# Kernel optimization log

Hardware: AMD Instinct MI355X
Metric: run time of the kernel (lower is better)

The kernel has to match this reference:

```python
import jax, jax.numpy as jnp
import numpy as np

N = 20480          # total points (single cloud, batch id 0)
C = 64             # in_channels
K = 16             # neighbors
CHUNK = 512        # knn_batch_size: query chunk for cdist
BN_EPS = 1e-5
# grid_size_options: [tower, background, line] x 3 axes
GRID_OPTIONS = np.array([[0.05, 0.05, 0.05],
                         [0.20, 0.20, 0.20],
                         [0.10, 0.10, 0.10]], dtype=np.float32)


def setup_inputs() -> dict:
    key = jax.random.key(0)
    k1, k2, k3, k4 = jax.random.split(key, 4)
    feat = jax.random.normal(k1, (N, C), jnp.float32)
    coord = jax.random.uniform(k2, (N, 3), jnp.float32)
    batch = jnp.zeros((N,), jnp.int32)
    fj_w1 = jax.random.normal(k3, (C, 32), jnp.float32) * 0.05
    fj_b1 = jnp.zeros((32,), jnp.float32)
    bn_gamma = jnp.ones((32,), jnp.float32)
    bn_beta = jnp.zeros((32,), jnp.float32)
    fj_w2 = jax.random.normal(k4, (32, 3), jnp.float32) * 0.05
    fj_b2 = jnp.zeros((3,), jnp.float32)
    return {"feat": feat, "coord": coord, "batch": batch,
            "fj_w1": fj_w1, "fj_b1": fj_b1, "bn_gamma": bn_gamma,
            "bn_beta": bn_beta, "fj_w2": fj_w2, "fj_b2": fj_b2}


def reference(feat, coord, batch, fj_w1, fj_b1, bn_gamma, bn_beta, fj_w2, fj_b2):
    # ---- chunked brute-force KNN (cdist + topk, self excluded) ----
    sq_all = jnp.sum(coord * coord, axis=-1)            # [N]
    col = jnp.arange(N)
    coords_chunks = coord.reshape(-1, CHUNK, 3)
    idx_chunks = jnp.arange(N).reshape(-1, CHUNK)

    def knn_chunk(args):
        cq, qi = args                                   # [CHUNK,3], [CHUNK]
        d2 = (jnp.sum(cq * cq, -1)[:, None] + sq_all[None, :]
              - 2.0 * (cq @ coord.T))                   # [CHUNK, N]
        d2 = jnp.maximum(d2, 1e-12)
        d2 = jnp.where(col[None, :] == qi[:, None], jnp.inf, d2)
        neg, idx = jax.lax.top_k(-d2, K)                # smallest-K (sqrt monotone)
        return jnp.sqrt(-neg), idx

    dists, idxs = jax.lax.map(jax.checkpoint(knn_chunk), (coords_chunks, idx_chunks))
    all_dist = dists.reshape(N, K)                      # [N, K]
    all_idx = idxs.reshape(N, K)                        # [N, K]

    # ---- per-point covariance of neighbor coords + 3x3 SVD (local PCA) ----
    nb = coord[all_idx]                                 # [N, K, 3]
    nc = nb - nb.mean(axis=1, keepdims=True)
    cov = jnp.einsum('nkd,nke->nde', nc, nc) / (K - 1)  # [N, 3, 3]
    S = jnp.linalg.svd(cov, compute_uv=False)           # descending, [N, 3]
    S_norm = S / (S.sum(axis=1, keepdims=True) + 1e-6)
    linearity = (S_norm[:, 0] - (S_norm[:, 1] + S_norm[:, 2]))[:, None]  # [N,1]

    mean_dist = all_dist.mean(axis=1, keepdims=True)
    density = 1.0 / (mean_dist + 1e-6)

    # ---- feature_judge MLP: Linear -> BatchNorm1d (train stats) -> ReLU -> Linear ----
    h = feat @ fj_w1 + fj_b1
    mu = h.mean(axis=0)
    var = h.var(axis=0)  # biased, as torch BN uses for normalization
    h = (h - mu) / jnp.sqrt(var + BN_EPS) * bn_gamma + bn_beta
    h = jax.nn.relu(h)
    probs = jax.nn.softmax(h @ fj_w2 + fj_b2, axis=1)   # [N, 3]

    tower_prob = (density * 2.0 + probs[:, 0:1]) / 3.0
    background_prob = (jnp.maximum(1.0 - linearity, 1.0 - density) + probs[:, 1:2]) / 3.0
    line_prob = (linearity * 2.0 + probs[:, 2:3]) / 3.0

    go = jnp.asarray(GRID_OPTIONS)
    line_grid = go[2] * jnp.array([1.0, 1.0, 5.0], jnp.float32)  # z-axis line grid *5
    grids = (tower_prob * go[0][None, :] + background_prob * go[1][None, :]
             + line_prob * line_grid[None, :] + 1e-6)   # [N, 3]
    return grids
```

## Files before the change

### kernel.cpp

```cpp
#include <hip/hip_runtime.h>

#define NPTS   20480
#define KNN    16
#define NSLOT  20
#define NCH    32
#define NFEAT  64
#define BN_EPS 1e-5f
#define AMB_EPS 2.6e-7f
#define GH     16
#define NCELL  (GH*GH*GH)
#define RHO0   2
#define NBLK   (NPTS / 256)
#define MLPBLK (NPTS / 32)
#define NGRP   (NPTS / 64)
#define NWAVE  4
#define NPAR   4

__device__ __forceinline__ unsigned med3u(unsigned a, unsigned b, unsigned c) {
    unsigned d;
    asm("v_med3_u32 %0, %1, %2, %3" : "=v"(d) : "v"(a), "v"(b), "v"(c));
    return d;
}

__device__ __forceinline__ float ref_d2_raw(float qx, float qy, float qz, float sqq,
                                            float cx, float cy, float cz, float sqc) {
    float dot = fmaf(qz, cz, fmaf(qy, cy, __fmul_rn(qx, cx)));
    float t   = __fadd_rn(sqq, sqc);
    return fmaf(-2.0f, dot, t);
}
__device__ __forceinline__ float ref_d2(float qx, float qy, float qz, float sqq,
                                        float cx, float cy, float cz, float sqc) {
    return fmaxf(ref_d2_raw(qx, qy, qz, sqq, cx, cy, cz, sqc), 1e-12f);
}

template <int STEP>
__device__ __forceinline__ void scan_range(const float4* __restrict__ spts,
                                           int c0, int c1, float4 qp, int self,
                                           unsigned* b) {
    for (int c = c0; c < c1; c += STEP) {
        float4 s = spts[c];
        float d2 = ref_d2_raw(qp.x, qp.y, qp.z, qp.w, s.x, s.y, s.z, s.w);
        unsigned key = (__float_as_uint(d2) & 0xFFFF8000u) | (unsigned)c;
        if (c == self) key = 0xFFFFFFFFu;
#pragma unroll
        for (int s2 = NSLOT - 1; s2 >= 1; --s2) b[s2] = med3u(key, b[s2 - 1], b[s2]);
        b[0] = min(key, b[0]);
    }
}

__global__ __launch_bounds__(256) void zero_cells(int* __restrict__ p) {
    p[blockIdx.x * 256 + threadIdx.x] = 0;
}

__global__ __launch_bounds__(256) void prep_mlp(const float* __restrict__ coord,
                                                float4* __restrict__ pts4,
                                                int* __restrict__ pcell,
                                                int* __restrict__ cnt,
                                                const float* __restrict__ feat,
                                                const float* __restrict__ w1,
                                                const float* __restrict__ b1,
                                                float* __restrict__ h_ws,
                                                float* __restrict__ partials) {
    if (blockIdx.x < NBLK) {
        int i = blockIdx.x * 256 + threadIdx.x;
        float x = coord[3 * i + 0], y = coord[3 * i + 1], z = coord[3 * i + 2];
        float sq = __fadd_rn(__fadd_rn(__fmul_rn(x, x), __fmul_rn(y, y)),
                             __fmul_rn(z, z));
        pts4[i] = make_float4(x, y, z, sq);
        int ix = min(GH - 1, max(0, (int)(x * (float)GH)));
        int iy = min(GH - 1, max(0, (int)(y * (float)GH)));
        int iz = min(GH - 1, max(0, (int)(z * (float)GH)));
        int cell = (iz * GH + iy) * GH + ix;
        pcell[i] = cell;
        atomicAdd(&cnt[cell], 1);
        return;
    }
    const int tid  = threadIdx.x;
    const int blk2 = blockIdx.x - NBLK;
    const int lane = tid & 63;
    const int wv   = tid >> 6;
    const int pt   = blk2 * 32 + (tid >> 3);
    const int k0   = (tid & 7) * 8;

    float h[NCH];
#pragma unroll
    for (int j = 0; j < NCH; ++j) h[j] = 0.f;
    const float4* f4 = reinterpret_cast<const float4*>(feat + (size_t)pt * NFEAT + k0);
#pragma unroll
    for (int c4 = 0; c4 < 2; ++c4) {
        float4 f = f4[c4];
        float fv[4] = {f.x, f.y, f.z, f.w};
#pragma unroll
        for (int e = 0; e < 4; ++e) {
            int c = k0 + c4 * 4 + e;
#pragma unroll
            for (int j = 0; j < NCH; ++j)
                h[j] = fmaf(fv[e], w1[c * NCH + j], h[j]);
        }
    }
#pragma unroll
    for (int j = 0; j < NCH; ++j) {
        h[j] += __shfl_xor(h[j], 1, 64);
        h[j] += __shfl_xor(h[j], 2, 64);
        h[j] += __shfl_xor(h[j], 4, 64);
        h[j] += b1[j];
    }
    if ((tid & 7) == 0) {
        float4* hd = reinterpret_cast<float4*>(h_ws + (size_t)pt * NCH);
#pragma unroll
        for (int j4 = 0; j4 < NCH / 4; ++j4)
            hd[j4] = make_float4(h[j4 * 4], h[j4 * 4 + 1],
                                 h[j4 * 4 + 2], h[j4 * 4 + 3]);
    }
    __shared__ float redS[4][NCH];
    __shared__ float redQ[4][NCH];
#pragma unroll
    for (int j = 0; j < NCH; ++j) {
        bool holder = (lane & 7) == 0;
        float v  = holder ? h[j] : 0.f;
        float vv = holder ? h[j] * h[j] : 0.f;
#pragma unroll
        for (int off = 8; off < 64; off <<= 1) {
            v  += __shfl_xor(v,  off, 64);
            vv += __shfl_xor(vv, off, 64);
        }
        if (lane == 0) { redS[wv][j] = v; redQ[wv][j] = vv; }
    }
    __syncthreads();
    if (tid < 64) {
        int j = tid;
        float r;
        if (j < NCH) r = redS[0][j] + redS[1][j] + redS[2][j] + redS[3][j];
        else {
            int jj = j - NCH;
            r = redQ[0][jj] + redQ[1][jj] + redQ[2][jj] + redQ[3][jj];
        }
        partials[blk2 * 64 + j] = r;
    }
}

__global__ __launch_bounds__(256) void scatter_pref(const float4* __restrict__ pts4,
                                                    const int* __restrict__ pcell,
                                                    const int* __restrict__ cnt,
                                                    int* __restrict__ cursor,
                                                    float4* __restrict__ spts,
                                                    int* __restrict__ sidx,
                                                    const float* __restrict__ partials,
                                                    float* __restrict__ mustats,
                                                    int* __restrict__ startArr) {
    const int tid = threadIdx.x;
    const int lane = tid & 63;
    if (blockIdx.x < NBLK) {
        __shared__ int chunks[256];
        __shared__ int sstart[NCELL];
        int local[16];
        int base = tid * 16, s = 0;
#pragma unroll
        for (int i = 0; i < 16; ++i) { local[i] = cnt[base + i]; s += local[i]; }
        chunks[tid] = s;
        __syncthreads();
        if (tid < 64) {
            int a0 = chunks[4 * tid + 0], a1 = chunks[4 * tid + 1];
            int a2 = chunks[4 * tid + 2], a3 = chunks[4 * tid + 3];
            int tot = a0 + a1 + a2 + a3;
            int inc = tot;
#pragma unroll
            for (int d = 1; d < 64; d <<= 1) {
                int t = __shfl_up(inc, d, 64);
                if (lane >= d) inc += t;
            }
            int excl = inc - tot;
            chunks[4 * tid + 0] = excl;
            chunks[4 * tid + 1] = excl + a0;
            chunks[4 * tid + 2] = excl + a0 + a1;
            chunks[4 * tid + 3] = excl + a0 + a1 + a2;
        }
        __syncthreads();
        int acc = chunks[tid];
#pragma unroll
        for (int i = 0; i < 16; ++i) { sstart[base + i] = acc; acc += local[i]; }
        __syncthreads();
        int i = blockIdx.x * 256 + tid;
        int c = pcell[i];
        int slot = sstart[c] + atomicAdd(&cursor[c], 1);
        spts[slot] = pts4[i];
        sidx[slot] = i;
        return;
    }
    if (tid < 64) {
        double s = 0.0;
        for (int bk = 0; bk < MLPBLK; ++bk) s += (double)partials[bk * 64 + lane];
        __shared__ double smu[NCH];
        if (lane < NCH) { double mu = s / (double)NPTS; smu[lane] = mu; mustats[lane] = (float)mu; }
        __syncthreads();
        if (lane >= NCH) {
            int jj = lane - NCH;
            double var = s / (double)NPTS - smu[jj] * smu[jj];
            mustats[lane] = (float)(1.0 / sqrt(var + (double)BN_EPS));
        }
    } else if (tid < 128) {
        __syncthreads();
        int base = lane * (NCELL / 64);
        int tot = 0;
        for (int i = 0; i < NCELL / 64; ++i) tot += cnt[base + i];
        int inc = tot;
#pragma unroll
        for (int d = 1; d < 64; d <<= 1) {
            int t = __shfl_up(inc, d, 64);
            if (lane >= d) inc += t;
        }
        int acc = inc - tot;
        for (int i = 0; i < NCELL / 64; ++i) { startArr[base + i] = acc; acc += cnt[base + i]; }
        if (lane == 63) startArr[NCELL] = acc;
    } else {
        __syncthreads();
    }
}

__global__ __launch_bounds__(256) void knn_scan(
    const float4* __restrict__ spts, const int* __restrict__ start,
    unsigned* __restrict__ quarterkeys) {
    __shared__ unsigned keysh[NWAVE * NSLOT][64];
    const int lane = threadIdx.x & 63;
    const int wv   = threadIdx.x >> 6;
    const int g    = blockIdx.x >> 2;
    const int par  = blockIdx.x & 3;
    const int slot = g * 64 + lane;
    const float4 qp = spts[slot];
    const int ix = min(GH - 1, max(0, (int)(qp.x * (float)GH)));
    const int iy = min(GH - 1, max(0, (int)(qp.y * (float)GH)));
    const int iz = min(GH - 1, max(0, (int)(qp.z * (float)GH)));

    unsigned b[NSLOT];
#pragma unroll
    for (int s = 0; s < NSLOT; ++s) b[s] = 0xFFFFFFFFu;
    {
        const int zlo = max(0, iz - RHO0), zhi = min(GH - 1, iz + RHO0);
        const int ylo = max(0, iy - RHO0), yhi = min(GH - 1, iy + RHO0);
        const int xlo = max(0, ix - RHO0), xhi = min(GH - 1, ix + RHO0);
        int r = 0;
        for (int cz = zlo; cz <= zhi; ++cz)
            for (int cy = ylo; cy <= yhi; ++cy) {
                if ((r & (NWAVE - 1)) == wv) {
                    const int rb = (cz * GH + cy) * GH;
                    int c0 = start[rb + xlo];
                    int c1 = start[rb + xhi + 1];
                    scan_range<NPAR>(spts, c0 + ((par - c0) & (NPAR - 1)), c1,
                                     qp, slot, b);
                }
                ++r;
            }
    }
#pragma unroll
    for (int s = 0; s < NSLOT; ++s) keysh[wv * NSLOT + s][lane] = b[s];
    __syncthreads();

    unsigned m[NSLOT];
    if (wv < 2) {
#pragma unroll
        for (int s = 0; s < NSLOT; ++s) m[s] = 0xFFFFFFFFu;
        for (int p2 = 2 * wv; p2 <= 2 * wv + 1; ++p2) {
#pragma unroll
            for (int s = 0; s < NSLOT; ++s) {
                unsigned key = keysh[p2 * NSLOT + s][lane];
#pragma unroll
                for (int t = NSLOT - 1; t >= 1; --t) m[t] = med3u(key, m[t - 1], m[t]);
                m[0] = min(key, m[0]);
            }
        }
    }
    __syncthreads();
    if (wv < 2) {
#pragma unroll
        for (int s = 0; s < NSLOT; ++s) keysh[wv * NSLOT + s][lane] = m[s];
    }
    __syncthreads();
    if (wv != 0) return;

#pragma unroll
    for (int s = 0; s < NSLOT; ++s) m[s] = 0xFFFFFFFFu;
    for (int p2 = 0; p2 < 2; ++p2) {
#pragma unroll
        for (int s = 0; s < NSLOT; ++s) {
            unsigned key = keysh[p2 * NSLOT + s][lane];
#pragma unroll
            for (int t = NSLOT - 1; t >= 1; --t) m[t] = med3u(key, m[t - 1], m[t]);
            m[0] = min(key, m[0]);
        }
    }
    unsigned* myh = quarterkeys + (size_t)(g * NPAR + par) * NSLOT * 64;
#pragma unroll
    for (int s = 0; s < NSLOT; ++s) myh[s * 64 + lane] = m[s];
}

__device__ void knn_stats(const float4* __restrict__ spts,
                          double qx, double qy, double qz,
                          const int* idx, const float* d2s,
                          double* den_out, double* lin_out) {
    double sx = 0, sy = 0, sz = 0;
    double sxx = 0, syy = 0, szz = 0, sxy = 0, sxz = 0, syz = 0;
    double dsum = 0;
#pragma unroll
    for (int s = 0; s < KNN; ++s) {
        float4 cp = spts[idx[s]];
        double ax = (double)cp.x - qx;
        double ay = (double)cp.y - qy;
        double az = (double)cp.z - qz;
        sx += ax; sy += ay; sz += az;
        sxx += ax * ax; syy += ay * ay; szz += az * az;
        sxy += ax * ay; sxz += ax * az; syz += ay * az;
        dsum += (double)sqrtf(d2s[s]);
    }
    const double invK  = 1.0 / KNN;
    const double invK1 = 1.0 / (KNN - 1);
    double mxx = sx * invK, myy = sy * invK, mzz = sz * invK;
    double cxx = (sxx - (double)KNN * mxx * mxx) * invK1;
    double cyy = (syy - (double)KNN * myy * myy) * invK1;
    double czz = (szz - (double)KNN * mzz * mzz) * invK1;
    double cxy = (sxy - (double)KNN * mxx * myy) * invK1;
    double cxz = (sxz - (double)KNN * mxx * mzz) * invK1;
    double cyz = (syz - (double)KNN * myy * mzz) * invK1;

    double T  = cxx + cyy + czz;
    double qq = T / 3.0;
    double b00 = cxx - qq, b11 = cyy - qq, b22 = czz - qq;
    double p2 = b00 * b00 + b11 * b11 + b22 * b22
              + 2.0 * (cxy * cxy + cxz * cxz + cyz * cyz);
    double lmax;
    if (p2 <= 1e-30) {
        lmax = qq;
    } else {
        double p = sqrt(p2 / 6.0);
        double detB = b00 * (b11 * b22 - cyz * cyz)
                    - cxy * (cxy * b22 - cyz * cxz)
                    + cxz * (cxy * cyz - b11 * cxz);
        double r = detB / (2.0 * p * p * p);
        r = fmin(1.0, fmax(-1.0, r));
        double phi = acos(r) / 3.0;
        lmax = qq + 2.0 * p * cos(phi);
    }
    *lin_out = (2.0 * lmax - T) / (T + 1e-6);
    *den_out = 1.0 / (dsum * invK + 1e-6);
}

__global__ __launch_bounds__(64) void knn_finalize(
    const float4* __restrict__ spts, const int* __restrict__ sidx,
    const int* __restrict__ start,   const unsigned* __restrict__ quarterkeys,
    const float* __restrict__ h_ws,  const float* __restrict__ gamma,
    const float* __restrict__ beta,  const float* __restrict__ w2,
    const float* __restrict__ b2,    const float* __restrict__ mustats,
    float* __restrict__ out) {
    const int lane = threadIdx.x;
    const int g    = blockIdx.x;
    const int slot = g * 64 + lane;
    const float4 qp = spts[slot];
    const int ix = min(GH - 1, max(0, (int)(qp.x * (float)GH)));
    const int iy = min(GH - 1, max(0, (int)(qp.y * (float)GH)));
    const int iz = min(GH - 1, max(0, (int)(qp.z * (float)GH)));

    unsigned m[NSLOT];
#pragma unroll
    for (int s = 0; s < NSLOT; ++s) m[s] = 0xFFFFFFFFu;
    for (int par = 0; par < NPAR; ++par) {
        const unsigned* ph = quarterkeys + (size_t)(g * NPAR + par) * NSLOT * 64;
#pragma unroll
        for (int s = 0; s < NSLOT; ++s) {
            unsigned key = ph[s * 64 + lane];
#pragma unroll
            for (int t = NSLOT - 1; t >= 1; --t) m[t] = med3u(key, m[t - 1], m[t]);
            m[0] = min(key, m[0]);
        }
    }

    const float h = 1.0f / (float)GH;
    int rho = RHO0;
    for (;;) {
        float b16f = __uint_as_float(m[16] & 0xFFFF8000u);
        float cov  = (float)(rho * rho) * (h * h);
        bool ok = (fmaf(b16f, 0.00390625f, b16f) + 1e-6f) <= cov;
        if (__all(ok) || rho >= GH - 1) break;
        ++rho;
        if (!ok) {
#pragma unroll
            for (int s = 0; s < NSLOT; ++s) m[s] = 0xFFFFFFFFu;
            const int zlo = max(0, iz - rho), zhi = min(GH - 1, iz + rho);
            const int ylo = max(0, iy - rho), yhi = min(GH - 1, iy + rho);
            const int xlo = max(0, ix - rho), xhi = min(GH - 1, ix + rho);
            for (int cz = zlo; cz <= zhi; ++cz)
                for (int cy = ylo; cy <= yhi; ++cy) {
                    const int rb = (cz * GH + cy) * GH;
                    scan_range<1>(spts, start[rb + xlo], start[rb + xhi + 1],
                                  qp, slot, m);
                }
        }
    }

    unsigned long long gk[KNN + 1];
#pragma unroll
    for (int s = 0; s < KNN + 1; ++s) gk[s] = ~0ull;
#pragma unroll
    for (int s = 0; s < NSLOT; ++s) {
        unsigned bs = m[s];
        int cs = min((int)(bs & 0x7FFFu), NPTS - 1);
        float4 cp = spts[cs];
        float d2 = ref_d2(qp.x, qp.y, qp.z, qp.w, cp.x, cp.y, cp.z, cp.w);
        unsigned long long kk =
            ((unsigned long long)__float_as_uint(d2) << 32) | (unsigned)cs;
        if (bs == 0xFFFFFFFFu) kk = ~0ull;
#pragma unroll
        for (int t = KNN; t >= 1; --t) {
            unsigned long long mn = (kk < gk[t]) ? kk : gk[t];
            gk[t] = (gk[t - 1] > mn) ? gk[t - 1] : mn;
        }
        gk[0] = (kk < gk[0]) ? kk : gk[0];
    }

    int   idxA[KNN];
    float d2A[KNN];
#pragma unroll
    for (int s = 0; s < KNN; ++s) {
        idxA[s] = (int)(gk[s] & 0xFFFFFFFFull);
        d2A[s]  = __uint_as_float((unsigned)(gk[s] >> 32));
    }
    float d16 = d2A[KNN - 1];
    float d17 = __uint_as_float((unsigned)(gk[KNN] >> 32));
    bool amb = (__fsub_rn(d17, d16) <= AMB_EPS);

    const double qx = (double)qp.x, qy = (double)qp.y, qz = (double)qp.z;
    double denA, linA;
    knn_stats(spts, qx, qy, qz, idxA, d2A, &denA, &linA);
    double den = denA, lin_d = linA;
    if (amb) {
        idxA[KNN - 1] = (int)(gk[KNN] & 0xFFFFFFFFull);
        d2A[KNN - 1]  = d17;
        double denB, linB;
        knn_stats(spts, qx, qy, qz, idxA, d2A, &denB, &linB);
        den = 0.5 * (denA + denB);
        lin_d = 0.5 * (linA + linB);
    }
    float dens = (float)den;
    float lin  = (float)lin_d;

    const int qi = sidx[slot];
    float hh[NCH];
    const float4* h4 = reinterpret_cast<const float4*>(h_ws + (size_t)qi * NCH);
#pragma unroll
    for (int j4 = 0; j4 < NCH / 4; ++j4) {
        float4 v = h4[j4];
        hh[j4 * 4 + 0] = v.x; hh[j4 * 4 + 1] = v.y;
        hh[j4 * 4 + 2] = v.z; hh[j4 * 4 + 3] = v.w;
    }
    float l0 = b2[0], l1 = b2[1], l2 = b2[2];
#pragma unroll
    for (int j = 0; j < NCH; ++j) {
        float xn = (hh[j] - mustats[j]) * mustats[NCH + j] * gamma[j] + beta[j];
        xn = fmaxf(xn, 0.f);
        l0 = fmaf(xn, w2[j * 3 + 0], l0);
        l1 = fmaf(xn, w2[j * 3 + 1], l1);
        l2 = fmaf(xn, w2[j * 3 + 2], l2);
    }
    float mx = fmaxf(l0, fmaxf(l1, l2));
    float e0 = expf(l0 - mx), e1 = expf(l1 - mx), e2 = expf(l2 - mx);
    float is = 1.f / (e0 + e1 + e2);
    float p0 = e0 * is, p1 = e1 * is, p2v = e2 * is;

    float tower = (dens * 2.f + p0) * (1.f / 3.f);
    float back  = (fmaxf(1.f - lin, 1.f - dens) + p1) * (1.f / 3.f);
    float line  = (lin * 2.f + p2v) * (1.f / 3.f);
    float gxy = fmaf(tower, 0.05f, fmaf(back, 0.20f, fmaf(line, 0.10f, 1e-6f)));
    float gz  = fmaf(tower, 0.05f, fmaf(back, 0.20f, fmaf(line, 0.50f, 1e-6f)));
    out[3 * qi + 0] = gxy;
    out[3 * qi + 1] = gxy;
    out[3 * qi + 2] = gz;
}

extern "C" void kernel_launch(void* const* d_in, const int* in_sizes, int n_in,
                              void* d_out, int out_size, void* d_ws, size_t ws_size,
                              hipStream_t stream) {
    const float* feat  = (const float*)d_in[0];
    const float* coord = (const float*)d_in[1];
    const float* w1    = (const float*)d_in[3];
    const float* b1    = (const float*)d_in[4];
    const float* gamma = (const float*)d_in[5];
    const float* beta  = (const float*)d_in[6];
    const float* w2    = (const float*)d_in[7];
    const float* b2    = (const float*)d_in[8];
    float* out = (float*)d_out;

    float4* pts4   = (float4*)d_ws;
    float4* spts   = pts4 + NPTS;
    int* sidx      = (int*)(spts + NPTS);
    int* pcell     = sidx + NPTS;
    int* cnt       = pcell + NPTS;
    int* cursor    = cnt + NCELL;
    int* startArr  = cursor + NCELL;
    unsigned* quarterkeys = (unsigned*)(startArr + NCELL + 8);
    float* partials  = (float*)(quarterkeys + (size_t)NPAR * NGRP * NSLOT * 64);
    float* mustats   = partials + MLPBLK * 64;
    float* h_ws      = mustats + 64;

    zero_cells<<<(2 * NCELL) / 256, 256, 0, stream>>>(cnt);
    prep_mlp<<<NBLK + MLPBLK, 256, 0, stream>>>(coord, pts4, pcell, cnt,
                                                feat, w1, b1, h_ws, partials);
    scatter_pref<<<NBLK + 1, 256, 0, stream>>>(pts4, pcell, cnt, cursor,
                                               spts, sidx, partials, mustats,
                                               startArr);
    knn_scan<<<NPAR * NGRP, 256, 0, stream>>>(spts, startArr, quarterkeys);
    knn_finalize<<<NGRP, 64, 0, stream>>>(spts, sidx, startArr, quarterkeys,
                                          h_ws, gamma, beta, w2, b2, mustats,
                                          out);
}
```

Measured before the change: 106.0 us.

## Restructure first MLP layer: stage features in LDS, split channels across waves

The feature-judge first linear layer now processes 64 points per block. Feature rows are staged into padded shared memory, and each wave handles a 16-channel slice for all 64 points, so the w1 reads are wave-uniform (scalar-loadable). The per-wave partial results are reduced through LDS, and the BN statistic partials are emitted as two 32-point halves to keep the partials layout unchanged. This aims to cut the redundant per-lane weight loads and the shuffle-heavy reduction of the old layout, at the cost of about 40KB of LDS per block, which may limit occupancy, and fewer blocks in the grid.

```diff
diff --git a/kernel.cpp b/kernel.cpp
--- a/kernel.cpp
+++ b/kernel.cpp
@@ -11,7 +11,8 @@
 #define NCELL  (GH*GH*GH)
 #define RHO0   2
 #define NBLK   (NPTS / 256)
-#define MLPBLK (NPTS / 32)
+#define MLPBLK 640
+#define MLPGRID (NPTS / 64)
 #define NGRP   (NPTS / 64)
 #define NWAVE  4
 #define NPAR   4
@@ -61,8 +62,12 @@
                                                 const float* __restrict__ b1,
                                                 float* __restrict__ h_ws,
                                                 float* __restrict__ partials) {
+    __shared__ float sfeat[64 * 65];
+    __shared__ float hpart[4][64][NCH + 1];
+    const int tid = threadIdx.x;
+
     if (blockIdx.x < NBLK) {
-        int i = blockIdx.x * 256 + threadIdx.x;
+        int i = blockIdx.x * 256 + tid;
         float x = coord[3 * i + 0], y = coord[3 * i + 1], z = coord[3 * i + 2];
         float sq = __fadd_rn(__fadd_rn(__fmul_rn(x, x), __fmul_rn(y, y)),
                              __fmul_rn(z, z));
@@ -75,67 +80,84 @@
         atomicAdd(&cnt[cell], 1);
         return;
     }
-    const int tid  = threadIdx.x;
-    const int blk2 = blockIdx.x - NBLK;
+    const int blk  = blockIdx.x - NBLK;
     const int lane = tid & 63;
-    const int wv   = tid >> 6;
-    const int pt   = blk2 * 32 + (tid >> 3);
-    const int k0   = (tid & 7) * 8;
+    const int wv   = __builtin_amdgcn_readfirstlane(tid >> 6);
+
+    const float4* fsrc = reinterpret_cast<const float4*>(feat + (size_t)blk * 64 * NFEAT);
+#pragma unroll
+    for (int it = 0; it < 4; ++it) {
+        float4 v = fsrc[it * 256 + tid];
+        int f = it * 1024 + tid * 4;
+        int pt = f >> 6, c = f & 63;
+        sfeat[pt * 65 + c + 0] = v.x;
+        sfeat[pt * 65 + c + 1] = v.y;
+        sfeat[pt * 65 + c + 2] = v.z;
+        sfeat[pt * 65 + c + 3] = v.w;
+    }
+    __syncthreads();
+
+    float hA[NCH], hB[NCH];
+#pragma unroll
+    for (int j = 0; j < NCH; ++j) { hA[j] = 0.f; hB[j] = 0.f; }
+    const int cbase = wv * 16;
+#pragma unroll
+    for (int cc = 0; cc < 16; ++cc) {
+        int c = cbase + cc;
+        float fv = sfeat[lane * 65 + c];
+        const float* wrow = w1 + c * NCH;
+        if (cc < 8) {
+#pragma unroll
+            for (int j = 0; j < NCH; ++j) hA[j] = fmaf(fv, wrow[j], hA[j]);
+        } else {
+#pragma unroll
+            for (int j = 0; j < NCH; ++j) hB[j] = fmaf(fv, wrow[j], hB[j]);
+        }
+    }
+#pragma unroll
+    for (int j = 0; j < NCH; ++j) hpart[wv][lane][j] = hA[j] + hB[j];
+    __syncthreads();
+    if (wv != 0) return;
 
     float h[NCH];
 #pragma unroll
-    for (int j = 0; j < NCH; ++j) h[j] = 0.f;
-    const float4* f4 = reinterpret_cast<const float4*>(feat + (size_t)pt * NFEAT + k0);
-#pragma unroll
-    for (int c4 = 0; c4 < 2; ++c4) {
-        float4 f = f4[c4];
-        float fv[4] = {f.x, f.y, f.z, f.w};
-#pragma unroll
-        for (int e = 0; e < 4; ++e) {
-            int c = k0 + c4 * 4 + e;
-#pragma unroll
-            for (int j = 0; j < NCH; ++j)
-                h[j] = fmaf(fv[e], w1[c * NCH + j], h[j]);
-        }
-    }
-#pragma unroll
     for (int j = 0; j < NCH; ++j) {
-        h[j] += __shfl_xor(h[j], 1, 64);
-        h[j] += __shfl_xor(h[j], 2, 64);
-        h[j] += __shfl_xor(h[j], 4, 64);
-        h[j] += b1[j];
-    }
-    if ((tid & 7) == 0) {
-        float4* hd = reinterpret_cast<float4*>(h_ws + (size_t)pt * NCH);
-#pragma unroll
-        for (int j4 = 0; j4 < NCH / 4; ++j4)
-            hd[j4] = make_float4(h[j4 * 4], h[j4 * 4 + 1],
-                                 h[j4 * 4 + 2], h[j4 * 4 + 3]);
-    }
-    __shared__ float redS[4][NCH];
-    __shared__ float redQ[4][NCH];
+        float q0 = hpart[0][lane][j], q1 = hpart[1][lane][j];
+        float q2 = hpart[2][lane][j], q3 = hpart[3][lane][j];
+        h[j] = (q0 + q1) + (q2 + q3) + 0.f;
+        h[j] = h[j] + b1[j];
+    }
+    float4* hd = reinterpret_cast<float4*>(h_ws + ((size_t)blk * 64 + lane) * NCH);
+#pragma unroll
+    for (int j4 = 0; j4 < NCH / 4; ++j4)
+        hd[j4] = make_float4(h[4 * j4], h[4 * j4 + 1], h[4 * j4 + 2], h[4 * j4 + 3]);
+
+    float myS0 = 0.f, myQ0 = 0.f, myS1 = 0.f, myQ1 = 0.f;
 #pragma unroll
     for (int j = 0; j < NCH; ++j) {
-        bool holder = (lane & 7) == 0;
-        float v  = holder ? h[j] : 0.f;
-        float vv = holder ? h[j] * h[j] : 0.f;
-#pragma unroll
-        for (int off = 8; off < 64; off <<= 1) {
-            v  += __shfl_xor(v,  off, 64);
-            vv += __shfl_xor(vv, off, 64);
-        }
-        if (lane == 0) { redS[wv][j] = v; redQ[wv][j] = vv; }
-    }
-    __syncthreads();
-    if (tid < 64) {
-        int j = tid;
-        float r;
-        if (j < NCH) r = redS[0][j] + redS[1][j] + redS[2][j] + redS[3][j];
-        else {
-            int jj = j - NCH;
-            r = redQ[0][jj] + redQ[1][jj] + redQ[2][jj] + redQ[3][jj];
-        }
-        partials[blk2 * 64 + j] = r;
+        float v = h[j], vv = h[j] * h[j];
+        v += __shfl_xor(v, 1, 64);  vv += __shfl_xor(vv, 1, 64);
+        v += __shfl_xor(v, 2, 64);  vv += __shfl_xor(vv, 2, 64);
+        v += __shfl_xor(v, 4, 64);  vv += __shfl_xor(vv, 4, 64);
+        float t0 = __shfl(v, 0, 64),  t1 = __shfl(v, 8, 64);
+        float t2 = __shfl(v, 16, 64), t3 = __shfl(v, 24, 64);
+        float t4 = __shfl(v, 32, 64), t5 = __shfl(v, 40, 64);
+        float t6 = __shfl(v, 48, 64), t7 = __shfl(v, 56, 64);
+        float u0 = __shfl(vv, 0, 64),  u1 = __shfl(vv, 8, 64);
+        float u2 = __shfl(vv, 16, 64), u3 = __shfl(vv, 24, 64);
+        float u4 = __shfl(vv, 32, 64), u5 = __shfl(vv, 40, 64);
+        float u6 = __shfl(vv, 48, 64), u7 = __shfl(vv, 56, 64);
+        float s0 = ((t0 + t1) + t2) + t3;
+        float s1 = ((t4 + t5) + t6) + t7;
+        float q0 = ((u0 + u1) + u2) + u3;
+        float q1 = ((u4 + u5) + u6) + u7;
+        if (lane == j) { myS0 = s0; myQ0 = q0; myS1 = s1; myQ1 = q1; }
+    }
+    if (lane < NCH) {
+        partials[(size_t)(2 * blk) * 64 + lane]            = myS0;
+        partials[(size_t)(2 * blk) * 64 + NCH + lane]      = myQ0;
+        partials[(size_t)(2 * blk + 1) * 64 + lane]        = myS1;
+        partials[(size_t)(2 * blk + 1) * 64 + NCH + lane]  = myQ1;
     }
 }
 
@@ -500,8 +522,8 @@
     float* h_ws      = mustats + 64;
 
     zero_cells<<<(2 * NCELL) / 256, 256, 0, stream>>>(cnt);
-    prep_mlp<<<NBLK + MLPBLK, 256, 0, stream>>>(coord, pts4, pcell, cnt,
-                                                feat, w1, b1, h_ws, partials);
+    prep_mlp<<<NBLK + MLPGRID, 256, 0, stream>>>(coord, pts4, pcell, cnt,
+                                                 feat, w1, b1, h_ws, partials);
     scatter_pref<<<NBLK + 1, 256, 0, stream>>>(pts4, pcell, cnt, cursor,
                                                spts, sidx, partials, mustats,
                                                startArr);
```

Result: faster. 87.87 us (-17.1%).
